# Optimization experiments

Hardware: AMD Instinct MI355X
Metric: run time of the kernel (lower is better)

The kernel has to match this reference:

```python
import jax, jax.numpy as jnp
import numpy as np

B, S, D = 32, 576, 768
G = 24  # sqrt(S)
TEMP = 0.01


def grid_sample_bilinear_zeros(img, grid):
    # img: (B,C,H,W), grid: (B,Hg,Wg,2) in [-1,1]; torch F.grid_sample,
    # mode='bilinear', padding_mode='zeros', align_corners=False
    Bn, C, H, W = img.shape
    gx, gy = grid[..., 0], grid[..., 1]
    ix = ((gx + 1.0) * W - 1.0) * 0.5
    iy = ((gy + 1.0) * H - 1.0) * 0.5
    x0 = jnp.floor(ix); y0 = jnp.floor(iy)
    x1 = x0 + 1.0;      y1 = y0 + 1.0
    wx1 = ix - x0; wx0 = 1.0 - wx1
    wy1 = iy - y0; wy0 = 1.0 - wy1

    def gather(xi, yi):
        valid = (xi >= 0) & (xi <= W - 1) & (yi >= 0) & (yi <= H - 1)
        xc = jnp.clip(xi, 0, W - 1).astype(jnp.int32)
        yc = jnp.clip(yi, 0, H - 1).astype(jnp.int32)
        vals = jax.vmap(lambda im, y, x: im[:, y, x])(img, yc, xc)  # (B,C,Hg,Wg)
        return vals * valid.astype(img.dtype)[:, None, :, :]

    return (gather(x0, y0) * (wx0 * wy0)[:, None]
            + gather(x1, y0) * (wx1 * wy0)[:, None]
            + gather(x0, y1) * (wx0 * wy1)[:, None]
            + gather(x1, y1) * (wx1 * wy1)[:, None])


def key_finder_net(h, W1, b1, W2, b2, W3, b3):
    # fc1 -> relu -> fc2 -> relu -> fc3 -> tanh
    h = jax.nn.relu(h @ W1 + b1)
    h = jax.nn.relu(h @ W2 + b2)
    return jnp.tanh(h @ W3 + b3)


def setup_inputs() -> dict:
    key = jax.random.key(0)
    ks = jax.random.split(key, 16)
    sd = 1.0 / np.sqrt(D)
    inp = {
        'x': jax.random.normal(ks[0], (B, S, D), dtype=jnp.float32),
        'indices': jax.random.randint(ks[1], (B, S), 0, S),
        'Wq': jax.random.normal(ks[2], (D, D), dtype=jnp.float32) * sd,
        'bq': jnp.zeros((D,), jnp.float32),
        'Wk': jax.random.normal(ks[3], (D, D), dtype=jnp.float32) * sd,
        'bk': jnp.zeros((D,), jnp.float32),
        'Wv': jax.random.normal(ks[4], (D, D), dtype=jnp.float32) * sd,
        'bv': jnp.zeros((D,), jnp.float32),
        'W1': jax.random.normal(ks[5], (2 * D, 60), dtype=jnp.float32) / np.sqrt(2 * D),
        'b1': jnp.zeros((60,), jnp.float32),
        'W2': jax.random.normal(ks[6], (60, 60), dtype=jnp.float32) / np.sqrt(60),
        'b2': jnp.zeros((60,), jnp.float32),
        'W3': jax.random.normal(ks[7], (60, 2), dtype=jnp.float32) / np.sqrt(60),
        'b3': jnp.zeros((2,), jnp.float32),
    }
    return inp


def reference(x, indices, Wq, bq, Wk, bk, Wv, bv, W1, b1, W2, b2, W3, b3):
    q = x @ Wq + bq  # (B,S,D)
    k = x @ Wk + bk
    v = x @ Wv + bv

    sample = key_finder_net(jnp.concatenate([q, k], axis=2), W1, b1, W2, b2, W3, b3)  # (B,S,2)
    # torch: cat((sample_x, sample_y), dim=1).reshape(B,G,G,2)
    flat = jnp.concatenate([sample[:, :, 0], sample[:, :, 1]], axis=1)  # (B,2S)
    grid = flat.reshape(B, G, G, 2)

    k_img = jnp.transpose(k, (0, 2, 1)).reshape(B, D, G, G)
    v_img = jnp.transpose(v, (0, 2, 1)).reshape(B, D, G, G)

    sk = grid_sample_bilinear_zeros(k_img, grid)  # (B,D,G,G)
    sv = grid_sample_bilinear_zeros(v_img, grid)
    sampled_key = jnp.transpose(sk.reshape(B, D, G * G), (0, 2, 1))   # (B,S,D)
    sampled_value = jnp.transpose(sv.reshape(B, D, G * G), (0, 2, 1))

    scores = jnp.sum(q * sampled_key, axis=-1)  # (B,S)
    return jax.nn.sigmoid(TEMP * scores)[..., None] * sampled_value
```

## Files before the change

### kernel.cpp

```cpp
#include <hip/hip_runtime.h>

typedef _Float16 f16;
typedef _Float16 f16x8 __attribute__((ext_vector_type(8)));
typedef _Float16 f16x4 __attribute__((ext_vector_type(4)));
typedef float f32x4 __attribute__((ext_vector_type(4)));
typedef float f32x16 __attribute__((ext_vector_type(16)));

constexpr int NB = 32, NS = 576, ND = 768, NG = 24;
constexpr int M_TOT = NB * NS;
constexpr int N_TOT = 3 * ND;

__global__ __launch_bounds__(256) void cast_w_t_kernel(const float* __restrict__ Wq,
                                                       const float* __restrict__ Wk,
                                                       const float* __restrict__ Wv,
                                                       f16* __restrict__ WT) {
  __shared__ float tile[64][65];
  int bt = blockIdx.x;
  int ntile = bt / 12, ktile = bt % 12;
  const float* src = (ntile < 12) ? Wq : ((ntile < 24) ? Wk : Wv);
  int n0 = (ntile % 12) * 64, k0 = ktile * 64;
  int cc = threadIdx.x & 63, rr = threadIdx.x >> 6;
#pragma unroll
  for (int i = 0; i < 16; i++) {
    int k = rr + i * 4;
    tile[cc][k] = src[(size_t)(k0 + k) * ND + n0 + cc];
  }
  __syncthreads();
#pragma unroll
  for (int i = 0; i < 16; i++) {
    int n = rr + i * 4;
    WT[(size_t)(ntile * 64 + n) * ND + k0 + cc] = (f16)tile[n][cc];
  }
}

__global__ __launch_bounds__(256) void wcT_kernel(const float* __restrict__ Wq,
                                                  const float* __restrict__ Wk,
                                                  const float* __restrict__ bq,
                                                  const float* __restrict__ bk,
                                                  const float* __restrict__ W1,
                                                  const float* __restrict__ b1,
                                                  f16* __restrict__ WcT_hi,
                                                  f16* __restrict__ WcT_lo,
                                                  float* __restrict__ bc) {
  if (blockIdx.x == 768) {
    int c = threadIdx.x;
    if (c < 60) {
      float acc = b1[c];
      for (int j = 0; j < ND; j++)
        acc += bq[j] * W1[j * 60 + c] + bk[j] * W1[(ND + j) * 60 + c];
      bc[c] = acc;
    }
    return;
  }
  __shared__ float part[4][64];
  int r = blockIdx.x;
  int wave = threadIdx.x >> 6, lane = threadIdx.x & 63;
  int c = (lane < 60) ? lane : 59;
  const float* wq = Wq + (size_t)r * ND;
  const float* wk = Wk + (size_t)r * ND;
  float acc = 0.f;
  int j0 = wave * 192;
  for (int j = j0; j < j0 + 192; j++)
    acc += wq[j] * W1[j * 60 + c] + wk[j] * W1[(ND + j) * 60 + c];
  part[wave][lane] = acc;
  __syncthreads();
  if (wave == 0 && lane < 60) {
    float v = part[0][lane] + part[1][lane] + part[2][lane] + part[3][lane];
    f16 hi = (f16)v;
    WcT_hi[(size_t)lane * ND + r] = hi;
    WcT_lo[(size_t)lane * ND + r] = (f16)(v - (float)hi);
  }
}

__global__ __launch_bounds__(256) void z1_fused_kernel(const float* __restrict__ x,
                                                       const f16* __restrict__ WcT_hi,
                                                       const f16* __restrict__ WcT_lo,
                                                       const float* __restrict__ bc,
                                                       const float* __restrict__ W2,
                                                       const float* __restrict__ b2,
                                                       const float* __restrict__ W3,
                                                       const float* __restrict__ b3,
                                                       f16* __restrict__ xb,
                                                       float* __restrict__ coords) {
  __shared__ float red[3][16][64];
  __shared__ float htile[16][60];
  int wave = threadIdx.x >> 6, lane = threadIdx.x & 63;
  int q = lane >> 4, r16 = lane & 15;
  int m0 = blockIdx.x * 16;
  int k0 = wave * 192;
  const float* xr = x + (size_t)(m0 + r16) * ND + k0;
  f16* xbr = xb + (size_t)(m0 + r16) * ND + k0;

  f32x4 acc[4];
#pragma unroll
  for (int nf = 0; nf < 4; nf++) acc[nf] = 0.f;

  for (int kk = 0; kk < 192; kk += 32) {
    int ko = kk + q * 8;
    float4 v0 = *(const float4*)(xr + ko);
    float4 v1 = *(const float4*)(xr + ko + 4);
    f16x8 a_hi, a_lo;
    float xv[8] = {v0.x, v0.y, v0.z, v0.w, v1.x, v1.y, v1.z, v1.w};
#pragma unroll
    for (int j = 0; j < 8; j++) {
      f16 h = (f16)xv[j];
      a_hi[j] = h;
      a_lo[j] = (f16)(xv[j] - (float)h);
    }
    *(f16x8*)(xbr + ko) = a_hi;
    f16x8 b_hi[4], b_lo[4];
#pragma unroll
    for (int nf = 0; nf < 4; nf++) {
      size_t off = (size_t)(nf * 16 + r16) * ND + k0 + ko;
      b_hi[nf] = *(const f16x8*)(WcT_hi + off);
      b_lo[nf] = *(const f16x8*)(WcT_lo + off);
    }
#pragma unroll
    for (int nf = 0; nf < 4; nf++) {
      acc[nf] = __builtin_amdgcn_mfma_f32_16x16x32_f16(a_hi, b_hi[nf], acc[nf], 0, 0, 0);
      acc[nf] = __builtin_amdgcn_mfma_f32_16x16x32_f16(a_lo, b_hi[nf], acc[nf], 0, 0, 0);
      acc[nf] = __builtin_amdgcn_mfma_f32_16x16x32_f16(a_hi, b_lo[nf], acc[nf], 0, 0, 0);
    }
  }

  if (wave > 0) {
#pragma unroll
    for (int nf = 0; nf < 4; nf++)
#pragma unroll
      for (int r = 0; r < 4; r++) red[wave - 1][nf * 4 + r][lane] = acc[nf][r];
  }
  __syncthreads();
  if (wave == 0) {
#pragma unroll
    for (int nf = 0; nf < 4; nf++) {
      int col = nf * 16 + r16;
      if (col < 60) {
        float bcv = bc[col];
#pragma unroll
        for (int r = 0; r < 4; r++) {
          float v = acc[nf][r] + red[0][nf * 4 + r][lane] + red[1][nf * 4 + r][lane]
                  + red[2][nf * 4 + r][lane] + bcv;
          htile[q * 4 + r][col] = fmaxf(v, 0.f);
        }
      }
    }
  }
  __syncthreads();

  int c = (lane < 60) ? lane : 59;
  float b2v = b2[c];
  float w30 = W3[c * 2 + 0], w31 = W3[c * 2 + 1];
#pragma unroll
  for (int rr = 0; rr < 4; rr++) {
    int row = wave * 4 + rr;
    float acc2 = b2v;
    for (int j = 0; j < 60; j++) acc2 = fmaf(htile[row][j], W2[j * 60 + c], acc2);
    float h2 = fmaxf(acc2, 0.f);
    float p0 = (lane < 60) ? h2 * w30 : 0.f;
    float p1 = (lane < 60) ? h2 * w31 : 0.f;
#pragma unroll
    for (int o = 32; o > 0; o >>= 1) { p0 += __shfl_down(p0, o); p1 += __shfl_down(p1, o); }
    if (lane == 0) {
      float s0 = tanhf(p0 + b3[0]);
      float s1 = tanhf(p1 + b3[1]);
      int m = m0 + row;
      int b = m / NS, s = m % NS;
      float* cb = coords + (size_t)b * (2 * NS);
      cb[(s >> 1) * 2 + (s & 1)] = s0;
      cb[(288 + (s >> 1)) * 2 + (s & 1)] = s1;
    }
  }
}

__device__ __forceinline__ void async_copy16(const f16* g, f16* l) {
  __builtin_amdgcn_global_load_lds((const __attribute__((address_space(1))) void*)g,
                                   (__attribute__((address_space(3))) void*)l, 16, 0, 0);
}

__global__ __launch_bounds__(256) void gemm_kernel(const f16* __restrict__ A,
                                                   const f16* __restrict__ Bt,
                                                   const float* __restrict__ bq,
                                                   const float* __restrict__ bk,
                                                   const float* __restrict__ bv,
                                                   f16* __restrict__ C) {
  constexpr int BM = 128, BK = 64;
  __shared__ __align__(16) f16 sA[BM * BK];
  __shared__ __align__(16) f16 sB[BM * BK];

  int bm = blockIdx.x % (M_TOT / BM);
  int bn = blockIdx.x / (M_TOT / BM);
  int tid = threadIdx.x;
  int wave = tid >> 6, lane = tid & 63;
  int wm = (wave >> 1) * 64, wn = (wave & 1) * 64;
  int m0 = bm * BM, n0 = bn * BM;

  int srow = tid >> 3;
  int gchunk = ((tid & 7) ^ (srow & 7)) * 8;

  f32x16 acc[2][2];
#pragma unroll
  for (int i = 0; i < 2; i++)
#pragma unroll
    for (int j = 0; j < 2; j++) acc[i][j] = 0.f;

  int r32 = lane & 31, q2 = lane >> 5;

  for (int kk = 0; kk < ND; kk += BK) {
#pragma unroll
    for (int ps = 0; ps < 4; ps++) {
      async_copy16(A + (size_t)(m0 + ps * 32 + srow) * ND + kk + gchunk, sA + ps * 2048 + tid * 8);
      async_copy16(Bt + (size_t)(n0 + ps * 32 + srow) * ND + kk + gchunk, sB + ps * 2048 + tid * 8);
    }
    __syncthreads();

#pragma unroll
    for (int ks = 0; ks < 4; ks++) {
      f16x8 aF[2], bF[2];
#pragma unroll
      for (int mt = 0; mt < 2; mt++) {
        int R = wm + mt * 32 + r32;
        aF[mt] = *(const f16x8*)(sA + R * 64 + (((ks * 2 + q2) ^ (R & 7)) * 8));
      }
#pragma unroll
      for (int nt = 0; nt < 2; nt++) {
        int R = wn + nt * 32 + r32;
        bF[nt] = *(const f16x8*)(sB + R * 64 + (((ks * 2 + q2) ^ (R & 7)) * 8));
      }
#pragma unroll
      for (int mt = 0; mt < 2; mt++)
#pragma unroll
        for (int nt = 0; nt < 2; nt++)
          acc[mt][nt] = __builtin_amdgcn_mfma_f32_32x32x16_f16(bF[nt], aF[mt], acc[mt][nt], 0, 0, 0);
    }
    __syncthreads();
  }

#pragma unroll
  for (int mt = 0; mt < 2; mt++) {
    int gm = m0 + wm + mt * 32 + r32;
#pragma unroll
    for (int nt = 0; nt < 2; nt++) {
#pragma unroll
      for (int g = 0; g < 4; g++) {
        int gn0 = n0 + wn + nt * 32 + 8 * g + 4 * q2;
        const float* bp = (gn0 < ND) ? (bq + gn0)
                        : ((gn0 < 2 * ND) ? (bk + gn0 - ND) : (bv + gn0 - 2 * ND));
        float4 bias = *(const float4*)bp;
        f16x4 o;
        o[0] = (f16)(acc[mt][nt][4 * g + 0] + bias.x);
        o[1] = (f16)(acc[mt][nt][4 * g + 1] + bias.y);
        o[2] = (f16)(acc[mt][nt][4 * g + 2] + bias.z);
        o[3] = (f16)(acc[mt][nt][4 * g + 3] + bias.w);
        *(f16x4*)(C + (size_t)gm * N_TOT + gn0) = o;
      }
    }
  }
}

__global__ __launch_bounds__(256) void sample_kernel(const f16* __restrict__ qkv,
                                                     const float* __restrict__ coords,
                                                     float* __restrict__ out) {
  int wave = threadIdx.x >> 6, t = threadIdx.x & 63;
  int x8 = blockIdx.x & 7;
  int i = blockIdx.x >> 3;
  int b = x8 * 4 + (i / 144);
  int p = (i % 144) * 4 + wave;

  float gx = coords[(size_t)b * (2 * NS) + p * 2 + 0];
  float gy = coords[(size_t)b * (2 * NS) + p * 2 + 1];
  float ix = ((gx + 1.f) * (float)NG - 1.f) * 0.5f;
  float iy = ((gy + 1.f) * (float)NG - 1.f) * 0.5f;
  float x0f = floorf(ix), y0f = floorf(iy);
  float wx1 = ix - x0f, wx0 = 1.f - wx1;
  float wy1 = iy - y0f, wy0 = 1.f - wy1;
  int x0 = (int)x0f, y0 = (int)y0f, x1 = x0 + 1, y1 = y0 + 1;
  bool vx0 = (x0 >= 0) & (x0 <= NG - 1), vx1 = (x1 >= 0) & (x1 <= NG - 1);
  bool vy0 = (y0 >= 0) & (y0 <= NG - 1), vy1 = (y1 >= 0) & (y1 <= NG - 1);
  int cx0 = min(max(x0, 0), NG - 1), cx1 = min(max(x1, 0), NG - 1);
  int cy0 = min(max(y0, 0), NG - 1), cy1 = min(max(y1, 0), NG - 1);
  float w00 = wx0 * wy0 * ((vx0 && vy0) ? 1.f : 0.f);
  float w10 = wx1 * wy0 * ((vx1 && vy0) ? 1.f : 0.f);
  float w01 = wx0 * wy1 * ((vx0 && vy1) ? 1.f : 0.f);
  float w11 = wx1 * wy1 * ((vx1 && vy1) ? 1.f : 0.f);

  size_t base = (size_t)b * NS;
  const f16* r00 = qkv + (base + cy0 * NG + cx0) * N_TOT;
  const f16* r10 = qkv + (base + cy0 * NG + cx1) * N_TOT;
  const f16* r01 = qkv + (base + cy1 * NG + cx0) * N_TOT;
  const f16* r11 = qkv + (base + cy1 * NG + cx1) * N_TOT;
  const f16* qr  = qkv + (base + p) * N_TOT;

  int d0 = t * 12;
  float partial = 0.f;
  float outv[12];
#pragma unroll
  for (int ch = 0; ch < 3; ch++) {
    int d = d0 + ch * 4;
    f16x4 k00 = *(const f16x4*)(r00 + ND + d);
    f16x4 k10 = *(const f16x4*)(r10 + ND + d);
    f16x4 k01 = *(const f16x4*)(r01 + ND + d);
    f16x4 k11 = *(const f16x4*)(r11 + ND + d);
    f16x4 v00 = *(const f16x4*)(r00 + 2 * ND + d);
    f16x4 v10 = *(const f16x4*)(r10 + 2 * ND + d);
    f16x4 v01 = *(const f16x4*)(r01 + 2 * ND + d);
    f16x4 v11 = *(const f16x4*)(r11 + 2 * ND + d);
    f16x4 qv  = *(const f16x4*)(qr + d);
#pragma unroll
    for (int j = 0; j < 4; j++) {
      float sk = w00 * (float)k00[j] + w10 * (float)k10[j]
               + w01 * (float)k01[j] + w11 * (float)k11[j];
      float sv = w00 * (float)v00[j] + w10 * (float)v10[j]
               + w01 * (float)v01[j] + w11 * (float)v11[j];
      partial = fmaf((float)qv[j], sk, partial);
      outv[ch * 4 + j] = sv;
    }
  }
#pragma unroll
  for (int o = 32; o > 0; o >>= 1) partial += __shfl_down(partial, o);
  float score = __shfl(partial, 0);
  float sig = 1.f / (1.f + expf(-0.01f * score));
  float* orow = out + (size_t)(base + p) * ND;
#pragma unroll
  for (int ch = 0; ch < 3; ch++) {
    float4 st;
    st.x = sig * outv[ch * 4 + 0]; st.y = sig * outv[ch * 4 + 1];
    st.z = sig * outv[ch * 4 + 2]; st.w = sig * outv[ch * 4 + 3];
    *(float4*)(orow + d0 + ch * 4) = st;
  }
}

extern "C" void kernel_launch(void* const* d_in, const int* in_sizes, int n_in,
                              void* d_out, int out_size, void* d_ws, size_t ws_size,
                              hipStream_t stream) {
  const float* x  = (const float*)d_in[0];
  const float* Wq = (const float*)d_in[2];
  const float* bq = (const float*)d_in[3];
  const float* Wk = (const float*)d_in[4];
  const float* bk = (const float*)d_in[5];
  const float* Wv = (const float*)d_in[6];
  const float* bv = (const float*)d_in[7];
  const float* W1 = (const float*)d_in[8];
  const float* b1 = (const float*)d_in[9];
  const float* W2 = (const float*)d_in[10];
  const float* b2 = (const float*)d_in[11];
  const float* W3 = (const float*)d_in[12];
  const float* b3 = (const float*)d_in[13];
  float* out = (float*)d_out;

  char* ws = (char*)d_ws;
  f16*   xb     = (f16*)(ws);
  f16*   WT     = (f16*)(ws + 28311552);
  f16*   qkv    = (f16*)(ws + 31850496);
  f16*   WcT_hi = (f16*)(ws + 31850496);
  f16*   WcT_lo = (f16*)(ws + 31948800);
  float* bc     = (float*)(ws + 116969472);
  float* coords = (float*)(ws + 121393408);

  cast_w_t_kernel<<<dim3(432), dim3(256), 0, stream>>>(Wq, Wk, Wv, WT);
  wcT_kernel<<<dim3(769), dim3(256), 0, stream>>>(Wq, Wk, bq, bk, W1, b1, WcT_hi, WcT_lo, bc);
  z1_fused_kernel<<<dim3(M_TOT / 16), dim3(256), 0, stream>>>(x, WcT_hi, WcT_lo, bc,
                                                              W2, b2, W3, b3, xb, coords);
  gemm_kernel<<<dim3((M_TOT / 128) * (N_TOT / 128)), dim3(256), 0, stream>>>(xb, WT, bq, bk, bv, qkv);
  sample_kernel<<<dim3(M_TOT / 4), dim3(256), 0, stream>>>(qkv, coords, out);
  (void)in_sizes; (void)n_in; (void)out_size; (void)ws_size;
}
```

Baseline: 348.0 us.

## Remap GEMM workgroups across XCDs, refine LDS swizzle, coalesce sampler accesses

The GEMM block index is remapped so that consecutive workgroups, which are round-robined across the 8 XCDs, share M tiles within each XCD for better L2 reuse. The LDS XOR swizzle gains extra bits to reduce bank conflicts on the MFMA fragment reads. The sampling kernel changes each lane's channel mapping from 12 contiguous elements to strided 4-element chunks, so a wave's loads and stores coalesce. The bias block of the Wc kernel is also split across four waves with a shared-memory reduction instead of running serially on one wave.

```diff
diff --git a/kernel.cpp b/kernel.cpp
--- a/kernel.cpp
+++ b/kernel.cpp
@@ -42,24 +42,24 @@
                                                   f16* __restrict__ WcT_hi,
                                                   f16* __restrict__ WcT_lo,
                                                   float* __restrict__ bc) {
-  if (blockIdx.x == 768) {
-    int c = threadIdx.x;
-    if (c < 60) {
-      float acc = b1[c];
-      for (int j = 0; j < ND; j++)
-        acc += bq[j] * W1[j * 60 + c] + bk[j] * W1[(ND + j) * 60 + c];
-      bc[c] = acc;
-    }
-    return;
-  }
   __shared__ float part[4][64];
-  int r = blockIdx.x;
   int wave = threadIdx.x >> 6, lane = threadIdx.x & 63;
   int c = (lane < 60) ? lane : 59;
+  int j0 = wave * 192;
+  if (blockIdx.x == 768) {
+    float acc = 0.f;
+    for (int j = j0; j < j0 + 192; j++)
+      acc += bq[j] * W1[j * 60 + c] + bk[j] * W1[(ND + j) * 60 + c];
+    part[wave][lane] = acc;
+    __syncthreads();
+    if (wave == 0 && lane < 60)
+      bc[lane] = b1[lane] + part[0][lane] + part[1][lane] + part[2][lane] + part[3][lane];
+    return;
+  }
+  int r = blockIdx.x;
   const float* wq = Wq + (size_t)r * ND;
   const float* wk = Wk + (size_t)r * ND;
   float acc = 0.f;
-  int j0 = wave * 192;
   for (int j = j0; j < j0 + 192; j++)
     acc += wq[j] * W1[j * 60 + c] + wk[j] * W1[(ND + j) * 60 + c];
   part[wave][lane] = acc;
@@ -187,15 +187,16 @@
   __shared__ __align__(16) f16 sA[BM * BK];
   __shared__ __align__(16) f16 sB[BM * BK];
 
-  int bm = blockIdx.x % (M_TOT / BM);
-  int bn = blockIdx.x / (M_TOT / BM);
+  int orig = blockIdx.x;
+  int wg = (orig & 7) * 324 + (orig >> 3);
+  int bm = wg / 18, bn = wg % 18;
   int tid = threadIdx.x;
   int wave = tid >> 6, lane = tid & 63;
   int wm = (wave >> 1) * 64, wn = (wave & 1) * 64;
   int m0 = bm * BM, n0 = bn * BM;
 
   int srow = tid >> 3;
-  int gchunk = ((tid & 7) ^ (srow & 7)) * 8;
+  int gchunk = ((tid & 7) ^ (srow & 7) ^ (((srow >> 3) & 3) << 1)) * 8;
 
   f32x16 acc[2][2];
 #pragma unroll
@@ -204,6 +205,7 @@
     for (int j = 0; j < 2; j++) acc[i][j] = 0.f;
 
   int r32 = lane & 31, q2 = lane >> 5;
+  int fx = (r32 & 7) ^ (((r32 >> 3) & 3) << 1);
 
   for (int kk = 0; kk < ND; kk += BK) {
 #pragma unroll
@@ -219,12 +221,12 @@
 #pragma unroll
       for (int mt = 0; mt < 2; mt++) {
         int R = wm + mt * 32 + r32;
-        aF[mt] = *(const f16x8*)(sA + R * 64 + (((ks * 2 + q2) ^ (R & 7)) * 8));
+        aF[mt] = *(const f16x8*)(sA + R * 64 + (((ks * 2 + q2) ^ fx) * 8));
       }
 #pragma unroll
       for (int nt = 0; nt < 2; nt++) {
         int R = wn + nt * 32 + r32;
-        bF[nt] = *(const f16x8*)(sB + R * 64 + (((ks * 2 + q2) ^ (R & 7)) * 8));
+        bF[nt] = *(const f16x8*)(sB + R * 64 + (((ks * 2 + q2) ^ fx) * 8));
       }
 #pragma unroll
       for (int mt = 0; mt < 2; mt++)
@@ -290,12 +292,11 @@
   const f16* r11 = qkv + (base + cy1 * NG + cx1) * N_TOT;
   const f16* qr  = qkv + (base + p) * N_TOT;
 
-  int d0 = t * 12;
   float partial = 0.f;
   float outv[12];
 #pragma unroll
   for (int ch = 0; ch < 3; ch++) {
-    int d = d0 + ch * 4;
+    int d = ch * 256 + t * 4;
     f16x4 k00 = *(const f16x4*)(r00 + ND + d);
     f16x4 k10 = *(const f16x4*)(r10 + ND + d);
     f16x4 k01 = *(const f16x4*)(r01 + ND + d);
@@ -322,10 +323,11 @@
   float* orow = out + (size_t)(base + p) * ND;
 #pragma unroll
   for (int ch = 0; ch < 3; ch++) {
+    int d = ch * 256 + t * 4;
     float4 st;
     st.x = sig * outv[ch * 4 + 0]; st.y = sig * outv[ch * 4 + 1];
     st.z = sig * outv[ch * 4 + 2]; st.w = sig * outv[ch * 4 + 3];
-    *(float4*)(orow + d0 + ch * 4) = st;
+    *(float4*)(orow + d) = st;
   }
 }
 
```

After: 332.1 us (median of 2 runs). 4.6% less time.
